# Kernel tuning notes

Hardware: AMD Instinct MI355X
Metric: run time of the kernel (lower is better)

Reference implementation:

```python
import jax, jax.numpy as jnp
import numpy as np

N_HEAD = 16
N_KV_HEAD = 4
HD = 128
ROPE_THETA = 10000.0


def _rope_cos_sin(T, hd, dtype):
    inv_freq = 1.0 / (ROPE_THETA ** (jnp.arange(0, hd, 2, dtype=jnp.float32) / hd))  # [hd/2]
    ang = jnp.arange(T, dtype=jnp.float32)[:, None] * inv_freq[None, :]  # [T, hd/2]
    return jnp.cos(ang).astype(dtype), jnp.sin(ang).astype(dtype)


def _apply_rope(x, cos, sin):
    # x: [B, T, H, hd]; rotate interleaved (even, odd) pairs Llama-style
    x1 = x[..., 0::2]
    x2 = x[..., 1::2]
    c = cos[None, :, None, :]
    s = sin[None, :, None, :]
    o1 = x1 * c - x2 * s
    o2 = x1 * s + x2 * c
    return jnp.stack([o1, o2], axis=-1).reshape(x.shape)


def setup_inputs() -> dict:
    key = jax.random.key(0)
    k1, k2, k3 = jax.random.split(key, 3)
    B, T, C = 4, 2048, 2048
    x = jax.random.normal(k1, (B, T, C), dtype=jnp.float32)
    w_attn = jax.random.normal(k2, ((N_HEAD + 2 * N_KV_HEAD) * HD, C), dtype=jnp.float32) * (C ** -0.5)
    w_proj = jax.random.normal(k3, (C, C), dtype=jnp.float32) * (C ** -0.5)
    return {"x": x, "w_attn": w_attn, "w_proj": w_proj}


def reference(x, w_attn, w_proj):
    B, T, C = x.shape
    n_rep = N_HEAD // N_KV_HEAD
    qkv = x @ w_attn.T  # [B, T, (H + 2*Hkv)*hd]
    q, k, v = jnp.split(qkv, [N_HEAD * HD, (N_HEAD + N_KV_HEAD) * HD], axis=-1)
    q = q.reshape(B, T, N_HEAD, HD)
    k = k.reshape(B, T, N_KV_HEAD, HD)
    v = v.reshape(B, T, N_KV_HEAD, HD)
    cos, sin = _rope_cos_sin(T, HD, x.dtype)
    q = _apply_rope(q, cos, sin)
    k = _apply_rope(k, cos, sin)
    # GQA: repeat kv heads (repeat_interleave on head dim)
    k = jnp.repeat(k, n_rep, axis=2)
    v = jnp.repeat(v, n_rep, axis=2)
    # [B, H, T, hd]
    q = q.transpose(0, 2, 1, 3)
    k = k.transpose(0, 2, 1, 3)
    v = v.transpose(0, 2, 1, 3)
    att = jnp.einsum("bhqd,bhkd->bhqk", q, k) * (1.0 / jnp.sqrt(jnp.asarray(HD, x.dtype)))
    causal = jnp.tril(jnp.ones((T, T), dtype=bool))
    att = jnp.where(causal[None, None, :, :], att, jnp.asarray(-jnp.inf, att.dtype))
    att = jax.nn.softmax(att, axis=-1)
    y = jnp.einsum("bhqk,bhkd->bhqd", att, v)
    y = y.transpose(0, 2, 1, 3).reshape(B, T, C)
    return y @ w_proj.T
```

## Files before the change

kernel.cpp:

```cpp
#include <hip/hip_runtime.h>
#include <math.h>

#define NH   16
#define NKV  4
#define HD   128
#define BSZ  4
#define TLEN 2048
#define CDIM 2048
#define MROWS (BSZ*TLEN)

typedef short bf16x8 __attribute__((ext_vector_type(8)));
typedef float f32x4  __attribute__((ext_vector_type(4)));
typedef int   int4v  __attribute__((ext_vector_type(4)));

__device__ inline float bf2f(unsigned short h) {
  union { unsigned u; float f; } x; x.u = ((unsigned)h) << 16; return x.f;
}
__device__ inline unsigned short f2bf(float f) {
  union { float f; unsigned u; } x; x.f = f;
  unsigned u = x.u;
  return (unsigned short)((u + 0x7FFFu + ((u >> 16) & 1u)) >> 16);
}

__device__ inline void gload_lds16(const void* g, void* l) {
  __builtin_amdgcn_global_load_lds((const __attribute__((address_space(1))) void*)g,
                                   (__attribute__((address_space(3))) void*)l, 16, 0, 0);
}

__global__ void detect_kernel(const void* __restrict__ wproj, int* __restrict__ flag) {
  __shared__ int cnt;
  if (threadIdx.x == 0) cnt = 0;
  __syncthreads();
  const unsigned short* s = (const unsigned short*)wproj;
  unsigned short v = s[2 * threadIdx.x];
  int e = (v >> 7) & 0xFF;
  if (e >= 90 && e <= 141) atomicAdd(&cnt, 1);
  __syncthreads();
  if (threadIdx.x == 0) *flag = (cnt >= 192) ? 1 : 0;
}

__device__ inline void stage8(short* dst, const void* src, size_t eoff, int isbf) {
  if (isbf) {
    *(int4v*)dst = *(const int4v*)((const short*)src + eoff);
  } else {
    const f32x4* f = (const f32x4*)((const float*)src + eoff);
    f32x4 a = f[0], b = f[1];
    __align__(16) short t[8];
    t[0] = (short)f2bf(a[0]); t[1] = (short)f2bf(a[1]);
    t[2] = (short)f2bf(a[2]); t[3] = (short)f2bf(a[3]);
    t[4] = (short)f2bf(b[0]); t[5] = (short)f2bf(b[1]);
    t[6] = (short)f2bf(b[2]); t[7] = (short)f2bf(b[3]);
    *(int4v*)dst = *(int4v*)t;
  }
}

__global__ __launch_bounds__(256) void cvt_kernel(const void* __restrict__ src,
                                                  short* __restrict__ dst,
                                                  int n8, const int* __restrict__ flagp)
{
  const int fl = *flagp;
  const int i = blockIdx.x * 256 + threadIdx.x;
  if (i >= n8) return;
  __align__(16) short t[8];
  stage8(t, src, (size_t)i * 8, fl);
  *(int4v*)(dst + (size_t)i * 8) = *(int4v*)t;
}

template<int MODE>
__global__ __launch_bounds__(256) void gemm_bt(
    const short* __restrict__ A, const short* __restrict__ W,
    short* __restrict__ o0, short* __restrict__ o1, short* __restrict__ o2,
    float* __restrict__ o0f, const int* __restrict__ flagp)
{
  __shared__ __align__(16) short As[128*32];
  __shared__ __align__(16) short Bs[128*32];
  const int fl = *flagp;
  const int tid  = threadIdx.x;
  const int wave = tid >> 6;
  const int lane = tid & 63;
  const int cl   = lane & 15;
  const int quad = lane >> 4;
  const int nwgx = gridDim.x;
  int wg = (int)blockIdx.y * nwgx + (int)blockIdx.x;
  const int cpx = (nwgx * (int)gridDim.y) >> 3;
  wg = (wg & 7) * cpx + (wg >> 3);
  const int m0 = (wg / nwgx) * 128;
  const int n0 = (wg % nwgx) * 128;
  const int wr = (wave >> 1) * 64;
  const int wc = (wave & 1) * 64;
  const int K = CDIM;
  const int rq = tid >> 2;
  const int cq = (tid & 3) << 3;
  const short* Ap = A + (size_t)(m0 + rq) * K + cq;
  const short* Wp = W + (size_t)(n0 + rq) * K + cq;
  short* AsW = As + wave * 512;
  short* BsW = Bs + wave * 512;
  const size_t rowskip = (size_t)64 * K;

  f32x4 acc[4][4];
#pragma unroll
  for (int i = 0; i < 4; i++)
#pragma unroll
    for (int j = 0; j < 4; j++) acc[i][j] = (f32x4){0.f, 0.f, 0.f, 0.f};

  for (int k0 = 0; k0 < K; k0 += 32) {
    gload_lds16(Ap + k0,           AsW);
    gload_lds16(Ap + k0 + rowskip, AsW + 2048);
    gload_lds16(Wp + k0,           BsW);
    gload_lds16(Wp + k0 + rowskip, BsW + 2048);
    __syncthreads();
    bf16x8 af[4], bfr[4];
#pragma unroll
    for (int i = 0; i < 4; i++) af[i]  = *(const bf16x8*)(&As[(wr + i*16 + cl)*32 + quad*8]);
#pragma unroll
    for (int j = 0; j < 4; j++) bfr[j] = *(const bf16x8*)(&Bs[(wc + j*16 + cl)*32 + quad*8]);
#pragma unroll
    for (int i = 0; i < 4; i++)
#pragma unroll
      for (int j = 0; j < 4; j++)
        acc[i][j] = __builtin_amdgcn_mfma_f32_16x16x32_bf16(af[i], bfr[j], acc[i][j], 0, 0, 0);
    __syncthreads();
  }

#pragma unroll
  for (int i = 0; i < 4; i++) {
#pragma unroll
    for (int j = 0; j < 4; j++) {
#pragma unroll
      for (int r = 0; r < 4; r++) {
        const int gm = m0 + wr + i*16 + quad*4 + r;
        const int gn = n0 + wc + j*16 + cl;
        const float fv = acc[i][j][r];
        if (MODE == 1) {
          if (fl) o0[(size_t)gm * CDIM + gn] = (short)f2bf(fv);
          else    o0f[(size_t)gm * CDIM + gn] = fv;
        } else {
          const int b = gm >> 11;
          const int t = gm & (TLEN - 1);
          const int head = gn >> 7;
          const int d = gn & (HD - 1);
          const unsigned short h = f2bf(fv);
          if (head < 16) {
            o0[(((size_t)(b*NH + head) * TLEN + t) << 7) + d] = (short)h;
          } else if (head < 20) {
            o1[(((size_t)(b*NKV + (head-16)) * TLEN + t) << 7) + d] = (short)h;
          } else {
            o2[(((size_t)(b*NKV + (head-20)) * HD + d) << 11) + t] = (short)h;
          }
        }
      }
    }
  }
}

__global__ __launch_bounds__(256) void rope_kernel(short* __restrict__ qb,
                                                   short* __restrict__ kb)
{
  const int idx = blockIdx.x * 256 + threadIdx.x;
  const int per_plane = TLEN * 64;
  const int plane = idx / per_plane;
  const int rem = idx - plane * per_plane;
  const int t = rem >> 6;
  const int i = rem & 63;
  short* base = (plane < 64) ? (qb + (size_t)plane * (TLEN*HD))
                             : (kb + (size_t)(plane - 64) * (TLEN*HD));
  const size_t off = (size_t)t * HD + 2*i;
  const float x1 = bf2f((unsigned short)base[off]);
  const float x2 = bf2f((unsigned short)base[off+1]);
  const float inv = __expf(-0.14391156847064198f * (float)i);
  const float ang = (float)t * inv;
  float s, c;
  sincosf(ang, &s, &c);
  const float qscale = (plane < 64) ? 0.08838834764831845f : 1.0f;
  base[off]   = (short)f2bf((x1*c - x2*s) * qscale);
  base[off+1] = (short)f2bf((x1*s + x2*c) * qscale);
}

__device__ inline void stage_tiles(short* Ks, short* Vs,
                                   const short* Kp, const short* Vp,
                                   int k0, int tid, int wave) {
#pragma unroll
  for (int i = 0; i < 4; i++) {
    const int chunk = i*256 + tid;
    const int row = chunk >> 4;
    const int cc  = (chunk & 15) ^ (row & 7);
    gload_lds16(Kp + (size_t)(k0 + row)*HD + cc*8,
                Ks + ((i*256 + wave*64) << 3));
  }
#pragma unroll
  for (int i = 0; i < 4; i++) {
    const int chunk = i*256 + tid;
    const int row = chunk >> 3;
    const int cc  = (chunk & 7) ^ (row & 7);
    gload_lds16(Vp + (size_t)row*TLEN + k0 + cc*8,
                Vs + ((i*256 + wave*64) << 3));
  }
}

__global__ __launch_bounds__(256) void attn_kernel(
    const short* __restrict__ qb, const short* __restrict__ kb,
    const short* __restrict__ vtb, short* __restrict__ yb)
{
  __shared__ __align__(16) short Ks[2][64*128];
  __shared__ __align__(16) short Vs[2][128*64];
  __shared__ short Plds[4][16][64];
  const int tid  = threadIdx.x;
  const int wave = tid >> 6;
  const int lane = tid & 63;
  const int cl   = lane & 15;
  const int quad = lane >> 4;
  const int bh = blockIdx.y;
  const int b = bh >> 4, h = bh & 15;
  const int kvh = h >> 2;

  const short* Qp = qb  + (size_t)(b*NH  + h)   * TLEN * HD;
  const short* Kp = kb  + (size_t)(b*NKV + kvh) * TLEN * HD;
  const short* Vp = vtb + (size_t)(b*NKV + kvh) * HD * TLEN;
  short* Pw = &Plds[wave][0][0];
  const int swz = (cl & 7) << 3;

#pragma unroll 1
  for (int pass = 0; pass < 2; ++pass) {
    const int qi = pass ? (TLEN/64 - 1 - (int)blockIdx.x) : (int)blockIdx.x;
    const int q0 = qi * 64;
    const int ntiles = qi + 1;

    bf16x8 qf[4];
    const int qrow = q0 + wave*16 + cl;
#pragma unroll
    for (int s = 0; s < 4; s++)
      qf[s] = *(const bf16x8*)(Qp + (size_t)qrow*HD + s*32 + quad*8);

    f32x4 O[8];
#pragma unroll
    for (int d = 0; d < 8; d++) O[d] = (f32x4){0.f, 0.f, 0.f, 0.f};
    float m_i[4], l_i[4];
#pragma unroll
    for (int r = 0; r < 4; r++) { m_i[r] = -1e9f; l_i[r] = 0.f; }

    stage_tiles(Ks[0], Vs[0], Kp, Vp, 0, tid, wave);
    __syncthreads();
    int cur = 0;

    for (int kt = 0; kt < ntiles; kt++) {
      const int k0 = kt * 64;

      if (kt + 1 < ntiles)
        stage_tiles(Ks[cur^1], Vs[cur^1], Kp, Vp, k0 + 64, tid, wave);

      const short* Kt = Ks[cur];
      const short* Vt = Vs[cur];

      f32x4 S[4];
#pragma unroll
      for (int j = 0; j < 4; j++) S[j] = (f32x4){0.f, 0.f, 0.f, 0.f};
#pragma unroll
      for (int s = 0; s < 4; s++) {
        bf16x8 kfj[4];
#pragma unroll
        for (int j = 0; j < 4; j++)
          kfj[j] = *(const bf16x8*)(&Kt[(size_t)(j*16 + cl)*128 + ((((s*4 + quad) << 3) ^ swz))]);
#pragma unroll
        for (int j = 0; j < 4; j++)
          S[j] = __builtin_amdgcn_mfma_f32_16x16x32_bf16(qf[s], kfj[j], S[j], 0, 0, 0);
      }

      if (kt == ntiles - 1) {
#pragma unroll
        for (int j = 0; j < 4; j++) {
          const int col = k0 + j*16 + cl;
#pragma unroll
          for (int r = 0; r < 4; r++) {
            const int row = q0 + wave*16 + quad*4 + r;
            if (col > row) S[j][r] = -1e9f;
          }
        }
      }

      float pmax[4];
#pragma unroll
      for (int r = 0; r < 4; r++) {
        float mx = fmaxf(fmaxf(S[0][r], S[1][r]), fmaxf(S[2][r], S[3][r]));
#pragma unroll
        for (int off = 1; off < 16; off <<= 1) mx = fmaxf(mx, __shfl_xor(mx, off));
        pmax[r] = mx;
      }
      const int ok = (pmax[0] - m_i[0] <= 8.f) && (pmax[1] - m_i[1] <= 8.f) &&
                     (pmax[2] - m_i[2] <= 8.f) && (pmax[3] - m_i[3] <= 8.f);
      if (!__all(ok)) {
#pragma unroll
        for (int r = 0; r < 4; r++) {
          const float mnew = fmaxf(m_i[r], pmax[r]);
          const float alpha = __expf(m_i[r] - mnew);
          l_i[r] *= alpha;
          m_i[r] = mnew;
#pragma unroll
          for (int d = 0; d < 8; d++) O[d][r] *= alpha;
        }
      }
#pragma unroll
      for (int r = 0; r < 4; r++) {
        float rs = 0.f;
#pragma unroll
        for (int j = 0; j < 4; j++) {
          const float p = __expf(S[j][r] - m_i[r]);
          S[j][r] = p;
          rs += p;
        }
#pragma unroll
        for (int off = 1; off < 16; off <<= 1) rs += __shfl_xor(rs, off);
        l_i[r] += rs;
      }

#pragma unroll
      for (int j = 0; j < 4; j++)
#pragma unroll
        for (int r = 0; r < 4; r++) {
          const int row = quad*4 + r;
          int idx = row*64 + j*16 + cl;
          idx ^= (row & 7) << 3;
          Pw[idx] = (short)f2bf(S[j][r]);
        }

#pragma unroll
      for (int s2 = 0; s2 < 2; s2++) {
        int idx = cl*64 + s2*32 + quad*8;
        idx ^= (cl & 7) << 3;
        bf16x8 pf = *(const bf16x8*)(&Pw[idx]);
#pragma unroll
        for (int d = 0; d < 8; d++) {
          bf16x8 vfd = *(const bf16x8*)(&Vt[(size_t)(d*16 + cl)*64 + ((((s2*4 + quad) << 3) ^ swz))]);
          O[d] = __builtin_amdgcn_mfma_f32_16x16x32_bf16(pf, vfd, O[d], 0, 0, 0);
        }
      }

      __syncthreads();
      cur ^= 1;
    }

    float linv[4];
#pragma unroll
    for (int r = 0; r < 4; r++) linv[r] = 1.0f / l_i[r];
#pragma unroll
    for (int d = 0; d < 8; d++) {
#pragma unroll
      for (int r = 0; r < 4; r++) {
        const int t = q0 + wave*16 + quad*4 + r;
        yb[(size_t)(b*TLEN + t) * CDIM + h*HD + d*16 + cl] = (short)f2bf(O[d][r] * linv[r]);
      }
    }
  }
}

extern "C" void kernel_launch(void* const* d_in, const int* in_sizes, int n_in,
                              void* d_out, int out_size, void* d_ws, size_t ws_size,
                              hipStream_t stream)
{
  const void* x      = d_in[0];
  const void* w_attn = d_in[1];
  const void* w_proj = d_in[2];

  char* ws = (char*)d_ws;
  int*   flag = (int*)ws;
  short* qb  = (short*)(ws + (size_t) 1*1024*1024);
  short* kb  = (short*)(ws + (size_t)33*1024*1024);
  short* vtb = (short*)(ws + (size_t)41*1024*1024);
  short* yb  = (short*)(ws + (size_t)49*1024*1024);
  short* xb  = (short*)d_out;
  short* wab = (short*)((char*)d_out + (size_t)32*1024*1024);
  short* wpb = kb;

  dim3 blk(256);
  detect_kernel<<<1, blk, 0, stream>>>(w_proj, flag);
  cvt_kernel<<<dim3((MROWS*CDIM/8)/256), blk, 0, stream>>>(x, xb, MROWS*CDIM/8, flag);
  cvt_kernel<<<dim3((3072*CDIM/8)/256), blk, 0, stream>>>(w_attn, wab, 3072*CDIM/8, flag);
  gemm_bt<0><<<dim3(3072/128, MROWS/128), blk, 0, stream>>>(xb, wab, qb, kb, vtb, nullptr, flag);
  rope_kernel<<<dim3((80*TLEN*64)/256), blk, 0, stream>>>(qb, kb);
  attn_kernel<<<dim3(TLEN/128, BSZ*NH), blk, 0, stream>>>(qb, kb, vtb, yb);
  cvt_kernel<<<dim3((CDIM*CDIM/8)/256), blk, 0, stream>>>(w_proj, wpb, CDIM*CDIM/8, flag);
  gemm_bt<1><<<dim3(CDIM/128, MROWS/128), blk, 0, stream>>>(yb, wpb, (short*)d_out,
                                                            nullptr, nullptr, (float*)d_out, flag);
}
```

Baseline: 592.4 us.

## Use 128-row query tiles with 8 waves and compute row sums via MFMA

The attention kernel now uses 512 threads (8 waves) per block, so each block covers 128 query rows and each staged K/V tile is shared by twice as many waves, halving the global K/V traffic per query. The causal mask is applied to the last two key tiles. The per-row softmax denominator is now built by an extra MFMA against a vector of bf16 ones on the P tile, replacing the cross-lane shuffle reduction. This costs one extra MFMA per sub-step, means the denominator comes from bf16-rounded P (which arguably matches the numerator better), and halves the grid size, which may reduce occupancy balance.

```diff
diff --git a/kernel.cpp b/kernel.cpp
--- a/kernel.cpp
+++ b/kernel.cpp
@@ -180,30 +180,30 @@
                                    const short* Kp, const short* Vp,
                                    int k0, int tid, int wave) {
 #pragma unroll
-  for (int i = 0; i < 4; i++) {
-    const int chunk = i*256 + tid;
+  for (int i = 0; i < 2; i++) {
+    const int chunk = i*512 + tid;
     const int row = chunk >> 4;
     const int cc  = (chunk & 15) ^ (row & 7);
     gload_lds16(Kp + (size_t)(k0 + row)*HD + cc*8,
-                Ks + ((i*256 + wave*64) << 3));
-  }
-#pragma unroll
-  for (int i = 0; i < 4; i++) {
-    const int chunk = i*256 + tid;
+                Ks + ((i*512 + wave*64) << 3));
+  }
+#pragma unroll
+  for (int i = 0; i < 2; i++) {
+    const int chunk = i*512 + tid;
     const int row = chunk >> 3;
     const int cc  = (chunk & 7) ^ (row & 7);
     gload_lds16(Vp + (size_t)row*TLEN + k0 + cc*8,
-                Vs + ((i*256 + wave*64) << 3));
-  }
-}
-
-__global__ __launch_bounds__(256) void attn_kernel(
+                Vs + ((i*512 + wave*64) << 3));
+  }
+}
+
+__global__ __launch_bounds__(512, 4) void attn_kernel(
     const short* __restrict__ qb, const short* __restrict__ kb,
     const short* __restrict__ vtb, short* __restrict__ yb)
 {
   __shared__ __align__(16) short Ks[2][64*128];
   __shared__ __align__(16) short Vs[2][128*64];
-  __shared__ short Plds[4][16][64];
+  __shared__ short Plds[8][16][64];
   const int tid  = threadIdx.x;
   const int wave = tid >> 6;
   const int lane = tid & 63;
@@ -219,11 +219,15 @@
   short* Pw = &Plds[wave][0][0];
   const int swz = (cl & 7) << 3;
 
+  bf16x8 ones;
+#pragma unroll
+  for (int i = 0; i < 8; i++) ones[i] = (short)0x3F80;
+
 #pragma unroll 1
   for (int pass = 0; pass < 2; ++pass) {
-    const int qi = pass ? (TLEN/64 - 1 - (int)blockIdx.x) : (int)blockIdx.x;
-    const int q0 = qi * 64;
-    const int ntiles = qi + 1;
+    const int qi = pass ? (TLEN/128 - 1 - (int)blockIdx.x) : (int)blockIdx.x;
+    const int q0 = qi * 128;
+    const int ntiles = 2*qi + 2;
 
     bf16x8 qf[4];
     const int qrow = q0 + wave*16 + cl;
@@ -234,9 +238,10 @@
     f32x4 O[8];
 #pragma unroll
     for (int d = 0; d < 8; d++) O[d] = (f32x4){0.f, 0.f, 0.f, 0.f};
-    float m_i[4], l_i[4];
-#pragma unroll
-    for (int r = 0; r < 4; r++) { m_i[r] = -1e9f; l_i[r] = 0.f; }
+    f32x4 Ol = (f32x4){0.f, 0.f, 0.f, 0.f};
+    float m_i[4];
+#pragma unroll
+    for (int r = 0; r < 4; r++) m_i[r] = -1e9f;
 
     stage_tiles(Ks[0], Vs[0], Kp, Vp, 0, tid, wave);
     __syncthreads();
@@ -265,7 +270,7 @@
           S[j] = __builtin_amdgcn_mfma_f32_16x16x32_bf16(qf[s], kfj[j], S[j], 0, 0, 0);
       }
 
-      if (kt == ntiles - 1) {
+      if (kt >= ntiles - 2) {
 #pragma unroll
         for (int j = 0; j < 4; j++) {
           const int col = k0 + j*16 + cl;
@@ -292,25 +297,17 @@
         for (int r = 0; r < 4; r++) {
           const float mnew = fmaxf(m_i[r], pmax[r]);
           const float alpha = __expf(m_i[r] - mnew);
-          l_i[r] *= alpha;
+          Ol[r] *= alpha;
           m_i[r] = mnew;
 #pragma unroll
           for (int d = 0; d < 8; d++) O[d][r] *= alpha;
         }
       }
 #pragma unroll
-      for (int r = 0; r < 4; r++) {
-        float rs = 0.f;
-#pragma unroll
-        for (int j = 0; j < 4; j++) {
-          const float p = __expf(S[j][r] - m_i[r]);
-          S[j][r] = p;
-          rs += p;
-        }
-#pragma unroll
-        for (int off = 1; off < 16; off <<= 1) rs += __shfl_xor(rs, off);
-        l_i[r] += rs;
-      }
+      for (int r = 0; r < 4; r++)
+#pragma unroll
+        for (int j = 0; j < 4; j++)
+          S[j][r] = __expf(S[j][r] - m_i[r]);
 
 #pragma unroll
       for (int j = 0; j < 4; j++)
@@ -327,6 +324,7 @@
         int idx = cl*64 + s2*32 + quad*8;
         idx ^= (cl & 7) << 3;
         bf16x8 pf = *(const bf16x8*)(&Pw[idx]);
+        Ol = __builtin_amdgcn_mfma_f32_16x16x32_bf16(pf, ones, Ol, 0, 0, 0);
 #pragma unroll
         for (int d = 0; d < 8; d++) {
           bf16x8 vfd = *(const bf16x8*)(&Vt[(size_t)(d*16 + cl)*64 + ((((s2*4 + quad) << 3) ^ swz))]);
@@ -340,7 +338,7 @@
 
     float linv[4];
 #pragma unroll
-    for (int r = 0; r < 4; r++) linv[r] = 1.0f / l_i[r];
+    for (int r = 0; r < 4; r++) linv[r] = 1.0f / Ol[r];
 #pragma unroll
     for (int d = 0; d < 8; d++) {
 #pragma unroll
@@ -376,7 +374,7 @@
   cvt_kernel<<<dim3((3072*CDIM/8)/256), blk, 0, stream>>>(w_attn, wab, 3072*CDIM/8, flag);
   gemm_bt<0><<<dim3(3072/128, MROWS/128), blk, 0, stream>>>(xb, wab, qb, kb, vtb, nullptr, flag);
   rope_kernel<<<dim3((80*TLEN*64)/256), blk, 0, stream>>>(qb, kb);
-  attn_kernel<<<dim3(TLEN/128, BSZ*NH), blk, 0, stream>>>(qb, kb, vtb, yb);
+  attn_kernel<<<dim3(TLEN/256, BSZ*NH), dim3(512), 0, stream>>>(qb, kb, vtb, yb);
   cvt_kernel<<<dim3((CDIM*CDIM/8)/256), blk, 0, stream>>>(w_proj, wpb, CDIM*CDIM/8, flag);
   gemm_bt<1><<<dim3(CDIM/128, MROWS/128), blk, 0, stream>>>(yb, wpb, (short*)d_out,
                                                             nullptr, nullptr, (float*)d_out, flag);
```

New measurement: 553.7 us. 1.07x faster.
